# Kernel optimization log

Measured on AMD Instinct MI355X. Metric: run time of the kernel, lower is better.

The kernel has to match this reference:

```python
import jax, jax.numpy as jnp
import numpy as np
import math

B, N, W = 8, 2048, 512

def setup_inputs() -> dict:
    key0 = jax.random.key(0)
    ks = jax.random.split(key0, 6)
    return {
        "query": jax.random.normal(ks[0], (B, N, W), dtype=jnp.float32),
        "key":   jax.random.normal(ks[1], (B, N, W), dtype=jnp.float32),
        "W1": jax.random.normal(ks[2], (W, W), dtype=jnp.float32) * (1.0 / math.sqrt(W)),
        "b1": jax.random.normal(ks[3], (W,), dtype=jnp.float32) * 0.01,
        "W2": jax.random.normal(ks[4], (W, W), dtype=jnp.float32) * (1.0 / math.sqrt(W)),
        "b2": jax.random.normal(ks[5], (W,), dtype=jnp.float32) * 0.01,
    }

def _attn(q, k, v):
    # scores: [B, N, N]
    d_k = q.shape[-1]
    scores = jnp.einsum('bnd,bmd->bnm', q, k) / jnp.sqrt(jnp.asarray(d_k, q.dtype))
    p = jax.nn.softmax(scores, axis=-1)
    return jnp.einsum('bnm,bmd->bnd', p, v)

def reference(query, key, W1, b1, W2, b2):
    # nn.Linear: x @ W.T + b
    q = jnp.einsum('bnd,ed->bne', query, W1) + b1
    k = jnp.einsum('bnd,ed->bne', key, W2) + b2
    x1 = _attn(q, k, q)  # attention(query, key, query)
    x2 = _attn(k, q, k)  # attention(key, query, key)
    return jnp.concatenate((x1, x2), axis=1)  # [B, 2N, W]
```

## Files before the change

kernel.cpp:

```cpp
#include <hip/hip_runtime.h>
#include <hip/hip_bf16.h>
#include <stdint.h>

typedef unsigned short ushort_t;
typedef __attribute__((ext_vector_type(8))) short short8;
typedef __attribute__((ext_vector_type(4))) short short4v;
typedef __attribute__((ext_vector_type(4))) float f32x4;

__device__ inline ushort_t f2bf(float x) {
  uint32_t u = __float_as_uint(x);
  u += 0x7fffu + ((u >> 16) & 1u);
  return (ushort_t)(u >> 16);
}
__device__ inline float bfu2f(uint32_t h) { return __uint_as_float(h << 16); }

__device__ inline uint32_t pk2bf(float a, float b) {
  __hip_bfloat162 h = __float22bfloat162_rn(make_float2(a, b));
  union { __hip_bfloat162 h2; uint32_t u; } cv; cv.h2 = h; return cv.u;
}

__device__ inline void gload_lds16(const void* g, void* l) {
  __builtin_amdgcn_global_load_lds((const __attribute__((address_space(1))) uint32_t*)g,
                                   (__attribute__((address_space(3))) uint32_t*)l, 16, 0, 0);
}

__global__ __launch_bounds__(256) void linear_kernel(
    const float* __restrict__ query, const float* __restrict__ key,
    const float* __restrict__ W1, const float* __restrict__ b1,
    const float* __restrict__ W2, const float* __restrict__ b2,
    ushort_t* __restrict__ q_bf, ushort_t* __restrict__ k_bf,
    ushort_t* __restrict__ qT, ushort_t* __restrict__ kT)
{
  __shared__ __attribute__((aligned(16))) char smraw[34816];
  float*    smF = (float*)smraw;
  ushort_t* smU = (ushort_t*)smraw;

  int bx = blockIdx.x;
  int which = bx >> 9, r2 = bx & 511, ct = r2 & 3, rt = r2 >> 2;
  const float* X    = which ? key : query;
  const float* Wm   = which ? W2  : W1;
  const float* bias = which ? b2  : b1;
  ushort_t* OUT  = which ? k_bf : q_bf;
  ushort_t* OUTT = which ? kT   : qT;

  int t = threadIdx.x, w = t >> 6, lane = t & 63, g = lane >> 4, m = lane & 15;
  int wr = (w >> 1) * 64, wc = (w & 1) * 64;
  int sr = lane >> 3, sp = lane & 7, sc = sp ^ sr;

  f32x4 zero = {0.f, 0.f, 0.f, 0.f};
  f32x4 acc[4][4];
#pragma unroll
  for (int i = 0; i < 4; ++i)
#pragma unroll
    for (int j = 0; j < 4; ++j) acc[i][j] = zero;

  for (int d0 = 0; d0 < 512; d0 += 32) {
    __syncthreads();
#pragma unroll
    for (int i = 0; i < 8; ++i) {
      int qi = w * 8 + i;
      const float* gsrc;
      float* ldst;
      if (qi < 16) {
        gsrc = X + (size_t)(rt * 128 + qi * 8 + sr) * 512 + d0 + sc * 4;
        ldst = smF + qi * 256;
      } else {
        int s = qi - 16;
        gsrc = Wm + (size_t)(ct * 128 + s * 8 + sr) * 512 + d0 + sc * 4;
        ldst = smF + 4096 + s * 256;
      }
      gload_lds16(gsrc, ldst);
    }
    __syncthreads();

    short8 a4[4], b4[4];
#pragma unroll
    for (int i = 0; i < 4; ++i) {
      int row = wr + 16 * i + m, r8 = row & 7;
      int base = (row >> 3) * 256 + r8 * 32;
      f32x4 lo = *(const f32x4*)&smF[base + (((2 * g)     ^ r8) * 4)];
      f32x4 hi = *(const f32x4*)&smF[base + (((2 * g + 1) ^ r8) * 4)];
      union { uint32_t u[4]; short8 s; } fr;
      fr.u[0] = pk2bf(lo[0], lo[1]); fr.u[1] = pk2bf(lo[2], lo[3]);
      fr.u[2] = pk2bf(hi[0], hi[1]); fr.u[3] = pk2bf(hi[2], hi[3]);
      a4[i] = fr.s;
    }
#pragma unroll
    for (int j = 0; j < 4; ++j) {
      int row = wc + 16 * j + m, r8 = row & 7;
      int base = 4096 + (row >> 3) * 256 + r8 * 32;
      f32x4 lo = *(const f32x4*)&smF[base + (((2 * g)     ^ r8) * 4)];
      f32x4 hi = *(const f32x4*)&smF[base + (((2 * g + 1) ^ r8) * 4)];
      union { uint32_t u[4]; short8 s; } fr;
      fr.u[0] = pk2bf(lo[0], lo[1]); fr.u[1] = pk2bf(lo[2], lo[3]);
      fr.u[2] = pk2bf(hi[0], hi[1]); fr.u[3] = pk2bf(hi[2], hi[3]);
      b4[j] = fr.s;
    }
#pragma unroll
    for (int i = 0; i < 4; ++i)
#pragma unroll
      for (int j = 0; j < 4; ++j)
        acc[i][j] = __builtin_amdgcn_mfma_f32_16x16x32_bf16(a4[i], b4[j], acc[i][j], 0, 0, 0);
  }
  __syncthreads();

  float bw[4];
#pragma unroll
  for (int j = 0; j < 4; ++j) bw[j] = bias[ct * 128 + wc + 16 * j + m];

#pragma unroll
  for (int j = 0; j < 4; ++j)
#pragma unroll
    for (int i = 0; i < 4; ++i) {
      f32x4 c4 = acc[i][j];
#pragma unroll
      for (int rr = 0; rr < 4; ++rr)
        smU[(wr + 16 * i + 4 * g + rr) * 136 + wc + 16 * j + m] = f2bf(c4[rr] + bw[j]);
    }
  __syncthreads();
  {
    int row = t >> 1, half = t & 1;
    size_t gb = (size_t)(rt * 128 + row) * 512 + ct * 128 + half * 64;
#pragma unroll
    for (int i = 0; i < 8; ++i)
      *(short8*)(OUT + gb + i * 8) = *(const short8*)&smU[row * 136 + half * 64 + i * 8];
  }
  __syncthreads();

#pragma unroll
  for (int j = 0; j < 4; ++j)
#pragma unroll
    for (int i = 0; i < 4; ++i) {
      f32x4 c4 = acc[i][j];
      short4v tv;
#pragma unroll
      for (int rr = 0; rr < 4; ++rr) tv[rr] = (short)f2bf(c4[rr] + bw[j]);
      *(short4v*)&smU[(wc + 16 * j + m) * 136 + wr + 16 * i + 4 * g] = tv;
    }
  __syncthreads();
  {
    int cC = t >> 1, half = t & 1;
    size_t b_ = (size_t)(rt >> 4);
    size_t gb = b_ * (512 * 2048) + (size_t)(ct * 128 + cC) * 2048
              + (size_t)(rt & 15) * 128 + half * 64;
#pragma unroll
    for (int i = 0; i < 8; ++i)
      *(short8*)(OUTT + gb + i * 8) = *(const short8*)&smU[cC * 136 + half * 64 + i * 8];
  }
}

__global__ __launch_bounds__(512) void attn_kernel(
    const ushort_t* __restrict__ qb, const ushort_t* __restrict__ kb_,
    const ushort_t* __restrict__ qT, const ushort_t* __restrict__ kT,
    float* __restrict__ out)
{
  extern __shared__ ushort_t sm[];
  const float CEXP = 1.4426950408889634f / 22.62741699796952f;

  int bx = blockIdx.x;
  int group = bx & 15, mtile = bx >> 4;
  int b = group >> 1, att = group & 1;
  const ushort_t* Qp = (att ? kb_ : qb) + (size_t)b * (2048 * 512);
  const ushort_t* Kp = (att ? qb  : kb_) + (size_t)b * (2048 * 512);
  const ushort_t* Vt = (att ? kT  : qT)  + (size_t)b * (512 * 2048);

  int t = threadIdx.x, w = t >> 6, lane = t & 63, g = lane >> 4, m = lane & 15;
  int qrow = mtile * 128 + w * 16 + m;
  int sw8  = ((g ^ ((m >> 1) & 3)) * 8);
  int srow = lane >> 2;
  int soff = ((lane & 3) ^ ((lane >> 3) & 3)) * 8;

  short8 qf[16];
#pragma unroll
  for (int ks = 0; ks < 16; ++ks)
    qf[ks] = *(const short8*)(Qp + (size_t)qrow * 512 + ks * 32 + g * 8);

  f32x4 zero = {0.f, 0.f, 0.f, 0.f};
  f32x4 acc[32];
#pragma unroll
  for (int dt = 0; dt < 32; ++dt) acc[dt] = zero;
  float l = 0.f;

  auto stage = [&](int buf, int kb) {
    ushort_t* base = sm + buf * 32768;
    const int kbase = kb * 32;
#pragma unroll
    for (int i = 0; i < 4; ++i) {
      int qi = w * 4 + i, ks = qi >> 1, tt2 = qi & 1;
      const ushort_t* gsrc = Kp + (size_t)(kbase + tt2 * 16 + srow) * 512 + ks * 32 + soff;
      gload_lds16(gsrc, base + ks * 1024 + tt2 * 512);
    }
#pragma unroll
    for (int i = 0; i < 4; ++i) {
      int qi = w * 4 + i;
      const ushort_t* gsrc = Vt + (size_t)(qi * 16 + srow) * 2048 + kbase + soff;
      gload_lds16(gsrc, base + 16384 + qi * 512);
    }
  };

  stage(0, 0);

  for (int kb = 0; kb < 64; ++kb) {
    int cur = kb & 1;
    __syncthreads();
    if (kb + 1 < 64) stage(1 - cur, kb + 1);
    const ushort_t* base = sm + cur * 32768;

    f32x4 T0 = zero, T1 = zero;
#pragma unroll
    for (int ks = 0; ks < 16; ++ks) {
      short8 k0 = *(const short8*)&base[ks * 1024 +       m * 32 + sw8];
      short8 k1 = *(const short8*)&base[ks * 1024 + 512 + m * 32 + sw8];
      T0 = __builtin_amdgcn_mfma_f32_16x16x32_bf16(k0, qf[ks], T0, 0, 0, 0);
      T1 = __builtin_amdgcn_mfma_f32_16x16x32_bf16(k1, qf[ks], T1, 0, 0, 0);
    }

    uint32_t h[8];
#pragma unroll
    for (int r = 0; r < 4; ++r) {
      float e0 = __builtin_amdgcn_exp2f(T0[r] * CEXP);
      float e1 = __builtin_amdgcn_exp2f(T1[r] * CEXP);
      h[r]     = f2bf(e0);
      h[4 + r] = f2bf(e1);
      l += bfu2f(h[r]) + bfu2f(h[4 + r]);
    }
    int dw0 = (int)(h[0] | (h[1] << 16));
    int dw1 = (int)(h[2] | (h[3] << 16));
    int dw2 = (int)(h[4] | (h[5] << 16));
    int dw3 = (int)(h[6] | (h[7] << 16));

    int sA = ((2 * g) & 3) * 16 + m, sB = sA + 16;
    int A0 = __shfl(dw0, sA, 64), A1 = __shfl(dw1, sA, 64);
    int A2 = __shfl(dw2, sA, 64), A3 = __shfl(dw3, sA, 64);
    int B0 = __shfl(dw0, sB, 64), B1 = __shfl(dw1, sB, 64);
    int B2 = __shfl(dw2, sB, 64), B3 = __shfl(dw3, sB, 64);
    bool hi = (g >= 2);
    union { int i4[4]; short8 s; } pu;
    pu.i4[0] = hi ? A2 : A0; pu.i4[1] = hi ? A3 : A1;
    pu.i4[2] = hi ? B2 : B0; pu.i4[3] = hi ? B3 : B1;
    short8 pfrag = pu.s;

#pragma unroll
    for (int dt = 0; dt < 32; ++dt) {
      short8 vf = *(const short8*)&base[16384 + dt * 512 + m * 32 + sw8];
      acc[dt] = __builtin_amdgcn_mfma_f32_16x16x32_bf16(vf, pfrag, acc[dt], 0, 0, 0);
    }
  }

  l += __shfl_xor(l, 16, 64);
  l += __shfl_xor(l, 32, 64);
  float inv = 1.0f / l;
  size_t orow = (size_t)b * 4096 + (size_t)att * 2048 + mtile * 128 + w * 16 + m;
  float* obase = out + orow * 512;
#pragma unroll
  for (int dt = 0; dt < 32; ++dt) {
    f32x4 v = acc[dt] * inv;
    *(f32x4*)(obase + dt * 16 + g * 4) = v;
  }
}

extern "C" void kernel_launch(void* const* d_in, const int* in_sizes, int n_in,
                              void* d_out, int out_size, void* d_ws, size_t ws_size,
                              hipStream_t stream) {
  const float* query = (const float*)d_in[0];
  const float* key   = (const float*)d_in[1];
  const float* W1    = (const float*)d_in[2];
  const float* b1    = (const float*)d_in[3];
  const float* W2    = (const float*)d_in[4];
  const float* b2    = (const float*)d_in[5];
  float* out = (float*)d_out;

  ushort_t* ws   = (ushort_t*)d_ws;
  ushort_t* q_bf = ws;
  ushort_t* k_bf = ws + 8388608;
  ushort_t* qT   = ws + 16777216;
  ushort_t* kT   = ws + 25165824;

  (void)hipFuncSetAttribute((const void*)attn_kernel,
                            hipFuncAttributeMaxDynamicSharedMemorySize, 131072);

  linear_kernel<<<1024, 256, 0, stream>>>(query, key, W1, b1, W2, b2,
                                          q_bf, k_bf, qT, kT);
  attn_kernel<<<256, 512, 131072, stream>>>(q_bf, k_bf, qT, kT, out);
}
```

Measured before the change: 333.8 us.

## Double 16-row tiles per wave in attention, double-buffer linear loads

The attention kernel now runs 4 waves per block, and each wave processes two 16-row query tiles. Each K/V fragment read from LDS therefore feeds two MFMAs, and s_setprio is raised around the MFMA loops. The linear kernel gets double-buffered global-to-LDS staging in dynamic shared memory, plus a block index swizzle. The cost is high register use (two accumulator sets and two Q fragment sets) and only one wave per SIMD, which reduces latency hiding.

Measured after the change: 377.8 us. +13.2%, slower.

```diff
diff --git a/kernel.cpp b/kernel.cpp
--- a/kernel.cpp
+++ b/kernel.cpp
@@ -31,11 +31,13 @@
     ushort_t* __restrict__ q_bf, ushort_t* __restrict__ k_bf,
     ushort_t* __restrict__ qT, ushort_t* __restrict__ kT)
 {
-  __shared__ __attribute__((aligned(16))) char smraw[34816];
+  extern __shared__ __attribute__((aligned(16))) char smraw[];
   float*    smF = (float*)smraw;
   ushort_t* smU = (ushort_t*)smraw;
 
-  int bx = blockIdx.x;
+  int bx0 = blockIdx.x;
+  int bx = ((bx0 & 7) << 7) | (bx0 >> 3);
+
   int which = bx >> 9, r2 = bx & 511, ct = r2 & 3, rt = r2 >> 2;
   const float* X    = which ? key : query;
   const float* Wm   = which ? W2  : W1;
@@ -54,8 +56,8 @@
 #pragma unroll
     for (int j = 0; j < 4; ++j) acc[i][j] = zero;
 
-  for (int d0 = 0; d0 < 512; d0 += 32) {
-    __syncthreads();
+  auto stage = [&](int buf, int d0) {
+    float* dst = smF + buf * 8192;
 #pragma unroll
     for (int i = 0; i < 8; ++i) {
       int qi = w * 8 + i;
@@ -63,23 +65,31 @@
       float* ldst;
       if (qi < 16) {
         gsrc = X + (size_t)(rt * 128 + qi * 8 + sr) * 512 + d0 + sc * 4;
-        ldst = smF + qi * 256;
+        ldst = dst + qi * 256;
       } else {
         int s = qi - 16;
         gsrc = Wm + (size_t)(ct * 128 + s * 8 + sr) * 512 + d0 + sc * 4;
-        ldst = smF + 4096 + s * 256;
+        ldst = dst + 4096 + s * 256;
       }
       gload_lds16(gsrc, ldst);
     }
+  };
+
+  stage(0, 0);
+
+  for (int it = 0; it < 16; ++it) {
+    int cur = it & 1;
     __syncthreads();
+    if (it + 1 < 16) stage(1 - cur, (it + 1) * 32);
+    const float* bufF = smF + cur * 8192;
 
     short8 a4[4], b4[4];
 #pragma unroll
     for (int i = 0; i < 4; ++i) {
       int row = wr + 16 * i + m, r8 = row & 7;
       int base = (row >> 3) * 256 + r8 * 32;
-      f32x4 lo = *(const f32x4*)&smF[base + (((2 * g)     ^ r8) * 4)];
-      f32x4 hi = *(const f32x4*)&smF[base + (((2 * g + 1) ^ r8) * 4)];
+      f32x4 lo = *(const f32x4*)&bufF[base + (((2 * g)     ^ r8) * 4)];
+      f32x4 hi = *(const f32x4*)&bufF[base + (((2 * g + 1) ^ r8) * 4)];
       union { uint32_t u[4]; short8 s; } fr;
       fr.u[0] = pk2bf(lo[0], lo[1]); fr.u[1] = pk2bf(lo[2], lo[3]);
       fr.u[2] = pk2bf(hi[0], hi[1]); fr.u[3] = pk2bf(hi[2], hi[3]);
@@ -89,8 +99,8 @@
     for (int j = 0; j < 4; ++j) {
       int row = wc + 16 * j + m, r8 = row & 7;
       int base = 4096 + (row >> 3) * 256 + r8 * 32;
-      f32x4 lo = *(const f32x4*)&smF[base + (((2 * g)     ^ r8) * 4)];
-      f32x4 hi = *(const f32x4*)&smF[base + (((2 * g + 1) ^ r8) * 4)];
+      f32x4 lo = *(const f32x4*)&bufF[base + (((2 * g)     ^ r8) * 4)];
+      f32x4 hi = *(const f32x4*)&bufF[base + (((2 * g + 1) ^ r8) * 4)];
       union { uint32_t u[4]; short8 s; } fr;
       fr.u[0] = pk2bf(lo[0], lo[1]); fr.u[1] = pk2bf(lo[2], lo[3]);
       fr.u[2] = pk2bf(hi[0], hi[1]); fr.u[3] = pk2bf(hi[2], hi[3]);
@@ -149,7 +159,7 @@
   }
 }
 
-__global__ __launch_bounds__(512) void attn_kernel(
+__global__ __launch_bounds__(256, 1) void attn_kernel(
     const ushort_t* __restrict__ qb, const ushort_t* __restrict__ kb_,
     const ushort_t* __restrict__ qT, const ushort_t* __restrict__ kT,
     float* __restrict__ out)
@@ -165,56 +175,43 @@
   const ushort_t* Vt = (att ? kT  : qT)  + (size_t)b * (512 * 2048);
 
   int t = threadIdx.x, w = t >> 6, lane = t & 63, g = lane >> 4, m = lane & 15;
-  int qrow = mtile * 128 + w * 16 + m;
+  int qrowA = mtile * 128 + w * 32 + m;
+  int qrowB = qrowA + 16;
   int sw8  = ((g ^ ((m >> 1) & 3)) * 8);
   int srow = lane >> 2;
   int soff = ((lane & 3) ^ ((lane >> 3) & 3)) * 8;
 
-  short8 qf[16];
-#pragma unroll
-  for (int ks = 0; ks < 16; ++ks)
-    qf[ks] = *(const short8*)(Qp + (size_t)qrow * 512 + ks * 32 + g * 8);
+  short8 qfA[16], qfB[16];
+#pragma unroll
+  for (int ks = 0; ks < 16; ++ks) {
+    qfA[ks] = *(const short8*)(Qp + (size_t)qrowA * 512 + ks * 32 + g * 8);
+    qfB[ks] = *(const short8*)(Qp + (size_t)qrowB * 512 + ks * 32 + g * 8);
+  }
 
   f32x4 zero = {0.f, 0.f, 0.f, 0.f};
-  f32x4 acc[32];
-#pragma unroll
-  for (int dt = 0; dt < 32; ++dt) acc[dt] = zero;
-  float l = 0.f;
+  f32x4 accA[32], accB[32];
+#pragma unroll
+  for (int dt = 0; dt < 32; ++dt) { accA[dt] = zero; accB[dt] = zero; }
+  float lA = 0.f, lB = 0.f;
 
   auto stage = [&](int buf, int kb) {
     ushort_t* base = sm + buf * 32768;
     const int kbase = kb * 32;
 #pragma unroll
-    for (int i = 0; i < 4; ++i) {
-      int qi = w * 4 + i, ks = qi >> 1, tt2 = qi & 1;
+    for (int i = 0; i < 8; ++i) {
+      int qi = w * 8 + i, ks = qi >> 1, tt2 = qi & 1;
       const ushort_t* gsrc = Kp + (size_t)(kbase + tt2 * 16 + srow) * 512 + ks * 32 + soff;
       gload_lds16(gsrc, base + ks * 1024 + tt2 * 512);
     }
 #pragma unroll
-    for (int i = 0; i < 4; ++i) {
-      int qi = w * 4 + i;
+    for (int i = 0; i < 8; ++i) {
+      int qi = w * 8 + i;
       const ushort_t* gsrc = Vt + (size_t)(qi * 16 + srow) * 2048 + kbase + soff;
       gload_lds16(gsrc, base + 16384 + qi * 512);
     }
   };
 
-  stage(0, 0);
-
-  for (int kb = 0; kb < 64; ++kb) {
-    int cur = kb & 1;
-    __syncthreads();
-    if (kb + 1 < 64) stage(1 - cur, kb + 1);
-    const ushort_t* base = sm + cur * 32768;
-
-    f32x4 T0 = zero, T1 = zero;
-#pragma unroll
-    for (int ks = 0; ks < 16; ++ks) {
-      short8 k0 = *(const short8*)&base[ks * 1024 +       m * 32 + sw8];
-      short8 k1 = *(const short8*)&base[ks * 1024 + 512 + m * 32 + sw8];
-      T0 = __builtin_amdgcn_mfma_f32_16x16x32_bf16(k0, qf[ks], T0, 0, 0, 0);
-      T1 = __builtin_amdgcn_mfma_f32_16x16x32_bf16(k1, qf[ks], T1, 0, 0, 0);
-    }
-
+  auto softmax_relayout = [&](f32x4 T0, f32x4 T1, float& lsum) -> short8 {
     uint32_t h[8];
 #pragma unroll
     for (int r = 0; r < 4; ++r) {
@@ -222,13 +219,12 @@
       float e1 = __builtin_amdgcn_exp2f(T1[r] * CEXP);
       h[r]     = f2bf(e0);
       h[4 + r] = f2bf(e1);
-      l += bfu2f(h[r]) + bfu2f(h[4 + r]);
+      lsum += bfu2f(h[r]) + bfu2f(h[4 + r]);
     }
     int dw0 = (int)(h[0] | (h[1] << 16));
     int dw1 = (int)(h[2] | (h[3] << 16));
     int dw2 = (int)(h[4] | (h[5] << 16));
     int dw3 = (int)(h[6] | (h[7] << 16));
-
     int sA = ((2 * g) & 3) * 16 + m, sB = sA + 16;
     int A0 = __shfl(dw0, sA, 64), A1 = __shfl(dw1, sA, 64);
     int A2 = __shfl(dw2, sA, 64), A3 = __shfl(dw3, sA, 64);
@@ -238,24 +234,60 @@
     union { int i4[4]; short8 s; } pu;
     pu.i4[0] = hi ? A2 : A0; pu.i4[1] = hi ? A3 : A1;
     pu.i4[2] = hi ? B2 : B0; pu.i4[3] = hi ? B3 : B1;
-    short8 pfrag = pu.s;
-
+    return pu.s;
+  };
+
+  stage(0, 0);
+
+  for (int kb = 0; kb < 64; ++kb) {
+    int cur = kb & 1;
+    __syncthreads();
+    if (kb + 1 < 64) stage(1 - cur, kb + 1);
+    const ushort_t* base = sm + cur * 32768;
+
+    f32x4 T0A = zero, T1A = zero, T0B = zero, T1B = zero;
+    __builtin_amdgcn_s_setprio(1);
+#pragma unroll
+    for (int ks = 0; ks < 16; ++ks) {
+      short8 k0 = *(const short8*)&base[ks * 1024 +       m * 32 + sw8];
+      short8 k1 = *(const short8*)&base[ks * 1024 + 512 + m * 32 + sw8];
+      T0A = __builtin_amdgcn_mfma_f32_16x16x32_bf16(k0, qfA[ks], T0A, 0, 0, 0);
+      T1A = __builtin_amdgcn_mfma_f32_16x16x32_bf16(k1, qfA[ks], T1A, 0, 0, 0);
+      T0B = __builtin_amdgcn_mfma_f32_16x16x32_bf16(k0, qfB[ks], T0B, 0, 0, 0);
+      T1B = __builtin_amdgcn_mfma_f32_16x16x32_bf16(k1, qfB[ks], T1B, 0, 0, 0);
+    }
+    __builtin_amdgcn_s_setprio(0);
+
+    short8 pfragA = softmax_relayout(T0A, T1A, lA);
+    short8 pfragB = softmax_relayout(T0B, T1B, lB);
+
+    __builtin_amdgcn_s_setprio(1);
 #pragma unroll
     for (int dt = 0; dt < 32; ++dt) {
       short8 vf = *(const short8*)&base[16384 + dt * 512 + m * 32 + sw8];
-      acc[dt] = __builtin_amdgcn_mfma_f32_16x16x32_bf16(vf, pfrag, acc[dt], 0, 0, 0);
-    }
-  }
-
-  l += __shfl_xor(l, 16, 64);
-  l += __shfl_xor(l, 32, 64);
-  float inv = 1.0f / l;
-  size_t orow = (size_t)b * 4096 + (size_t)att * 2048 + mtile * 128 + w * 16 + m;
-  float* obase = out + orow * 512;
+      accA[dt] = __builtin_amdgcn_mfma_f32_16x16x32_bf16(vf, pfragA, accA[dt], 0, 0, 0);
+      accB[dt] = __builtin_amdgcn_mfma_f32_16x16x32_bf16(vf, pfragB, accB[dt], 0, 0, 0);
+    }
+    __builtin_amdgcn_s_setprio(0);
+  }
+
+  lA += __shfl_xor(lA, 16, 64);
+  lA += __shfl_xor(lA, 32, 64);
+  lB += __shfl_xor(lB, 16, 64);
+  lB += __shfl_xor(lB, 32, 64);
+  float invA = 1.0f / lA, invB = 1.0f / lB;
+  size_t orowA = (size_t)b * 4096 + (size_t)att * 2048 + mtile * 128 + w * 32 + m;
+  float* obaseA = out + orowA * 512;
+  float* obaseB = out + (orowA + 16) * 512;
 #pragma unroll
   for (int dt = 0; dt < 32; ++dt) {
-    f32x4 v = acc[dt] * inv;
-    *(f32x4*)(obase + dt * 16 + g * 4) = v;
+    f32x4 vA = accA[dt] * invA;
+    *(f32x4*)(obaseA + dt * 16 + g * 4) = vA;
+  }
+#pragma unroll
+  for (int dt = 0; dt < 32; ++dt) {
+    f32x4 vB = accB[dt] * invB;
+    *(f32x4*)(obaseB + dt * 16 + g * 4) = vB;
   }
 }
 
@@ -276,10 +308,12 @@
   ushort_t* qT   = ws + 16777216;
   ushort_t* kT   = ws + 25165824;
 
+  (void)hipFuncSetAttribute((const void*)linear_kernel,
+                            hipFuncAttributeMaxDynamicSharedMemorySize, 65536);
   (void)hipFuncSetAttribute((const void*)attn_kernel,
                             hipFuncAttributeMaxDynamicSharedMemorySize, 131072);
 
-  linear_kernel<<<1024, 256, 0, stream>>>(query, key, W1, b1, W2, b2,
-                                          q_bf, k_bf, qT, kT);
-  attn_kernel<<<256, 512, 131072, stream>>>(q_bf, k_bf, qT, kT, out);
-}
+  linear_kernel<<<1024, 256, 65536, stream>>>(query, key, W1, b1, W2, b2,
+                                              q_bf, k_bf, qT, kT);
+  attn_kernel<<<256, 256, 131072, stream>>>(q_bf, k_bf, qT, kT, out);
+}
```
